# Performance work log

Measured on AMD Instinct MI355X. Metric: run time of the kernel, lower is better.

Reference implementation:

```python
import jax, jax.numpy as jnp
import numpy as np

N_NODES = 50000
N_EDGES = 600000
IN_FEAT = 128
EDGE_DIM = 3
N_HEADS = 4
OUT_FEAT = 32  # per head; N_HEADS*OUT_FEAT == IN_FEAT -> residual_proj is Identity


def setup_inputs() -> dict:
    key = jax.random.key(0)
    ks = jax.random.split(key, 16)
    s = 0.05
    H, F = N_HEADS, OUT_FEAT
    return {
        "node_feats": jax.random.normal(ks[0], (N_NODES, IN_FEAT), jnp.float32),
        "edge_feat": jax.random.normal(ks[1], (N_EDGES, EDGE_DIM), jnp.float32),
        "src": jax.random.randint(ks[2], (N_EDGES,), 0, N_NODES),
        "dst": jax.random.randint(ks[3], (N_EDGES,), 0, N_NODES),
        "W_em1": jax.random.normal(ks[4], (EDGE_DIM, 2 * EDGE_DIM), jnp.float32) * s,
        "b_em1": jnp.zeros((2 * EDGE_DIM,), jnp.float32),
        "W_em2": jax.random.normal(ks[5], (2 * EDGE_DIM, EDGE_DIM), jnp.float32) * s,
        "b_em2": jnp.zeros((EDGE_DIM,), jnp.float32),
        "W_np": jax.random.normal(ks[6], (IN_FEAT, IN_FEAT), jnp.float32) * s,
        "b_np": jnp.zeros((IN_FEAT,), jnp.float32),
        "W_fc": jax.random.normal(ks[7], (IN_FEAT + EDGE_DIM, H * F), jnp.float32) * s,
        "attn_l": jax.random.normal(ks[8], (H, F), jnp.float32) * s,
        "attn_r": jax.random.normal(ks[9], (H, F), jnp.float32) * s,
        "gat_bias": jnp.zeros((H * F,), jnp.float32),
        "ln_gamma": jnp.ones((H * F,), jnp.float32),
        "ln_beta": jnp.zeros((H * F,), jnp.float32),
    }


def reference(node_feats, edge_feat, src, dst, W_em1, b_em1, W_em2, b_em2,
              W_np, b_np, W_fc, attn_l, attn_r, gat_bias, ln_gamma, ln_beta):
    N = node_feats.shape[0]
    H, F = attn_l.shape
    # edge MLP: Linear -> SiLU -> Linear
    e = jax.nn.silu(edge_feat @ W_em1 + b_em1) @ W_em2 + b_em2            # [E, ED]
    p = node_feats @ W_np + b_np                                          # [N, IN]
    src_in = jnp.concatenate([p[src], e], axis=1)                         # [E, IN+ED]
    dst_in = jnp.concatenate([p[dst], e], axis=1)                         # [E, IN+ED]
    temp = jnp.zeros((N, src_in.shape[1]), node_feats.dtype)
    temp = temp.at[src].add(src_in).at[dst].add(dst_in)                   # scatter_add x2
    # GATConv (eval mode: feat_drop/attn_drop are identity)
    h = (temp @ W_fc).reshape(N, H, F)                                    # [N, H, F]
    el = jnp.einsum('nhf,hf->nh', h, attn_l)                              # [N, H]
    er = jnp.einsum('nhf,hf->nh', h, attn_r)                              # [N, H]
    logits = jax.nn.leaky_relu(el[src] + er[dst], negative_slope=0.2)     # [E, H]
    # destination-wise edge softmax (stable)
    m = jax.ops.segment_max(logits, dst, num_segments=N)                  # [N, H]
    a = jnp.exp(logits - m[dst])                                          # [E, H]
    z = jax.ops.segment_sum(a, dst, num_segments=N)                       # [N, H]
    alpha = a / z[dst]                                                    # [E, H]
    msg = alpha[:, :, None] * h[src]                                      # [E, H, F]
    rst = jax.ops.segment_sum(msg, dst, num_segments=N)                   # [N, H, F]
    rst = rst + gat_bias.reshape(1, H, F)
    gat_out = rst.reshape(N, H * F)
    out = gat_out + node_feats                                            # residual (Identity proj)
    mu = out.mean(axis=-1, keepdims=True)
    var = out.var(axis=-1, keepdims=True)
    out = (out - mu) / jnp.sqrt(var + 1e-5) * ln_gamma + ln_beta          # LayerNorm
    return jax.nn.silu(out)
```

## Files before the change

### kernel.cpp

```cpp
#include <hip/hip_runtime.h>
#include <hip/hip_bf16.h>

#define IN_FEAT 128
#define N_HEADS 4
#define OUT_FEAT 32

typedef __attribute__((ext_vector_type(8))) short short8;
typedef __attribute__((ext_vector_type(4))) float floatx4;

__device__ __forceinline__ void bf16split(float x, short& hi, short& lo) {
    unsigned u = __float_as_uint(x);
    unsigned r = (u + 0x7FFFu + ((u >> 16) & 1u)) & 0xFFFF0000u;
    hi = (short)(r >> 16);
    float res = x - __uint_as_float(r);
    unsigned u2 = __float_as_uint(res);
    unsigned r2 = u2 + 0x7FFFu + ((u2 >> 16) & 1u);
    lo = (short)(r2 >> 16);
}

__device__ __forceinline__ unsigned short bf16rne(float x) {
    unsigned u = __float_as_uint(x);
    return (unsigned short)((u + 0x7FFFu + ((u >> 16) & 1u)) >> 16);
}

__global__ void edge_scatter_kernel(const float* __restrict__ ef,
                                    const int* __restrict__ src, const int* __restrict__ dst,
                                    const float* __restrict__ W1, const float* __restrict__ b1,
                                    const float* __restrict__ W2, const float* __restrict__ b2,
                                    float* __restrict__ nd, int* __restrict__ erank, int E) {
    int t = blockIdx.x * blockDim.x + threadIdx.x;
    int e = t >> 3;
    int sub = t & 7;
    if (e >= E) return;
    float x0 = ef[e * 3 + 0], x1 = ef[e * 3 + 1], x2 = ef[e * 3 + 2];
    float hbuf[6];
#pragma unroll
    for (int j = 0; j < 6; j++) {
        float v = x0 * W1[0 * 6 + j] + x1 * W1[1 * 6 + j] + x2 * W1[2 * 6 + j] + b1[j];
        hbuf[j] = v / (1.0f + __expf(-v));
    }
    int j = sub & 3;
    float val;
    if (j == 0) {
        val = 1.0f;
    } else {
        float v = b2[j - 1];
#pragma unroll
        for (int k = 0; k < 6; k++) v += hbuf[k] * W2[k * 3 + (j - 1)];
        val = v;
    }
    int side = sub >> 2;
    int node = side ? dst[e] : src[e];
    int slot = (side && j == 0) ? 4 : j;
    float old = atomicAdd(&nd[(size_t)node * 8 + slot], val);
    if (sub == 4) erank[e] = (int)old;
}

__global__ __launch_bounds__(1024) void scan1_kernel(const float* __restrict__ nd,
                                                     int* __restrict__ excl,
                                                     int* __restrict__ bsum, int N) {
    __shared__ int buf[1024];
    int t = threadIdx.x;
    int i = blockIdx.x * 1024 + t;
    int v = (i < N) ? (int)nd[(size_t)i * 8 + 4] : 0;
    buf[t] = v;
    __syncthreads();
    for (int d = 1; d < 1024; d <<= 1) {
        int x = (t >= d) ? buf[t - d] : 0;
        __syncthreads();
        buf[t] += x;
        __syncthreads();
    }
    if (i < N) excl[i] = buf[t] - v;
    if (t == 1023) bsum[blockIdx.x] = buf[1023];
}

__global__ __launch_bounds__(1024) void scan2_kernel(const int* __restrict__ bsum,
                                                     int* __restrict__ boff, int nb) {
    __shared__ int buf[1024];
    int t = threadIdx.x;
    int v = (t < nb) ? bsum[t] : 0;
    buf[t] = v;
    __syncthreads();
    for (int d = 1; d < 1024; d <<= 1) {
        int x = (t >= d) ? buf[t - d] : 0;
        __syncthreads();
        buf[t] += x;
        __syncthreads();
    }
    if (t < nb) boff[t] = buf[t] - v;
}

__global__ __launch_bounds__(1024) void scan3_kernel(const int* __restrict__ excl,
                                                     const int* __restrict__ boff,
                                                     int* __restrict__ off, int N, int E) {
    int i = blockIdx.x * 1024 + threadIdx.x;
    if (i < N) off[i] = excl[i] + boff[blockIdx.x];
    if (i == 0) off[N] = E;
}

__global__ void wcomb_kernel(const float* __restrict__ W_np, const float* __restrict__ W_fc,
                             const float* __restrict__ b_np,
                             short* __restrict__ WBh, short* __restrict__ WBl,
                             float* __restrict__ bvec) {
    int i = blockIdx.x;
    int o = threadIdx.x;
    float acc = 0.0f;
    for (int j = 0; j < 128; j++) acc += W_np[i * 128 + j] * W_fc[j * 128 + o];
    short hi, lo;
    bf16split(acc, hi, lo);
    int t    = o >> 4;
    int kk   = i >> 5;
    int lane = ((i >> 3) & 3) * 16 + (o & 15);
    int jj   = i & 7;
    int fi = ((t * 4 + kk) * 64 + lane) * 8 + jj;
    WBh[fi] = hi;
    WBl[fi] = lo;
    if (i == 0) {
        float bb = 0.0f;
        for (int j = 0; j < 128; j++) bb += b_np[j] * W_fc[j * 128 + o];
        bvec[o] = bb;
    }
}

__global__ __launch_bounds__(256) void binh_kernel(
        const int* __restrict__ src, const int* __restrict__ dst,
        const int* __restrict__ eoff, const int* __restrict__ erank,
        int* __restrict__ ssrc, int E,
        const float* __restrict__ nf,
        const short* __restrict__ WBh, const short* __restrict__ WBl,
        const float* __restrict__ bvec, const float* __restrict__ W_fc,
        const float* __restrict__ nd,
        const float* __restrict__ attn_l, const float* __restrict__ attn_r,
        unsigned short* __restrict__ h16,
        float* __restrict__ el, float* __restrict__ er, int N) {
    __shared__ short lWh[16384];
    __shared__ short lWl[16384];
    {
        const int4* s1 = (const int4*)WBh;
        const int4* s2 = (const int4*)WBl;
        int4* d1 = (int4*)lWh;
        int4* d2 = (int4*)lWl;
        for (int i = threadIdx.x; i < 2048; i += 256) { d1[i] = s1[i]; d2[i] = s2[i]; }
    }
    __syncthreads();

    {
        int stride = gridDim.x * 256;
#pragma unroll 4
        for (int e = blockIdx.x * 256 + threadIdx.x; e < E; e += stride) {
            ssrc[eoff[dst[e]] + erank[e]] = src[e];
        }
    }

    const int w = threadIdx.x >> 6, l = threadIdx.x & 63;
    const int lrow = l & 15, lhalf = l >> 4;
    const int n0 = blockIdx.x * 64 + w * 16;
    const int arow = n0 + lrow;

    short8 ah[4], al_[4];
#pragma unroll
    for (int kk = 0; kk < 4; kk++) {
        float v[8];
        if (arow < N) {
            const float* p = &nf[(size_t)arow * 128 + kk * 32 + lhalf * 8];
            float4 f0 = *(const float4*)p;
            float4 f1 = *(const float4*)(p + 4);
            v[0] = f0.x; v[1] = f0.y; v[2] = f0.z; v[3] = f0.w;
            v[4] = f1.x; v[5] = f1.y; v[6] = f1.z; v[7] = f1.w;
        } else {
#pragma unroll
            for (int j = 0; j < 8; j++) v[j] = 0.0f;
        }
#pragma unroll
        for (int j = 0; j < 8; j++) {
            short hi, lo;
            bf16split(v[j], hi, lo);
            ah[kk][j] = hi;
            al_[kk][j] = lo;
        }
    }

    floatx4 acc[8];
#pragma unroll
    for (int t = 0; t < 8; t++) acc[t] = (floatx4){0.f, 0.f, 0.f, 0.f};

#pragma unroll
    for (int t = 0; t < 8; t++) {
#pragma unroll
        for (int kk = 0; kk < 4; kk++) {
            int fi = ((t * 4 + kk) * 64 + l) * 8;
            short8 bh = *(const short8*)&lWh[fi];
            short8 bl = *(const short8*)&lWl[fi];
            acc[t] = __builtin_amdgcn_mfma_f32_16x16x32_bf16(ah[kk], bh, acc[t], 0, 0, 0);
            acc[t] = __builtin_amdgcn_mfma_f32_16x16x32_bf16(ah[kk], bl, acc[t], 0, 0, 0);
            acc[t] = __builtin_amdgcn_mfma_f32_16x16x32_bf16(al_[kk], bh, acc[t], 0, 0, 0);
        }
    }

    float bv[8], w0[8], w1[8], w2[8], alb[8], arb[8];
#pragma unroll
    for (int t = 0; t < 8; t++) {
        int o = t * 16 + lrow;
        bv[t] = bvec[o];
        w0[t] = W_fc[128 * 128 + o];
        w1[t] = W_fc[129 * 128 + o];
        w2[t] = W_fc[130 * 128 + o];
        alb[t] = attn_l[o];
        arb[t] = attn_r[o];
    }
#pragma unroll
    for (int r = 0; r < 4; r++) {
        int node = n0 + lhalf * 4 + r;
        bool valid = node < N;
        float dg = 0.f, e0 = 0.f, e1 = 0.f, e2 = 0.f;
        if (valid) {
            dg = nd[(size_t)node * 8 + 0] + nd[(size_t)node * 8 + 4];
            e0 = nd[(size_t)node * 8 + 1];
            e1 = nd[(size_t)node * 8 + 2];
            e2 = nd[(size_t)node * 8 + 3];
        }
        float pl[4] = {0.f, 0.f, 0.f, 0.f}, pr[4] = {0.f, 0.f, 0.f, 0.f};
#pragma unroll
        for (int t = 0; t < 8; t++) {
            float hv = dg * (acc[t][r] + bv[t]) + e0 * w0[t] + e1 * w1[t] + e2 * w2[t];
            if (valid) h16[(size_t)node * 128 + t * 16 + lrow] = bf16rne(hv);
            pl[t >> 1] += hv * alb[t];
            pr[t >> 1] += hv * arb[t];
        }
#pragma unroll
        for (int hd = 0; hd < 4; hd++) {
#pragma unroll
            for (int mask = 1; mask <= 8; mask <<= 1) {
                pl[hd] += __shfl_xor(pl[hd], mask);
                pr[hd] += __shfl_xor(pr[hd], mask);
            }
        }
        if (valid) {
            if (lrow < 4)      el[node * 4 + lrow]       = pl[lrow];
            else if (lrow < 8) er[node * 4 + (lrow - 4)] = pr[lrow - 4];
        }
    }
}

__global__ __launch_bounds__(256) void gather_kernel(
        const int* __restrict__ off, const int* __restrict__ sorted_src,
        const float* __restrict__ el, const float* __restrict__ er,
        const unsigned short* __restrict__ h16, const float* __restrict__ nf,
        const float* __restrict__ gat_bias, const float* __restrict__ gamma,
        const float* __restrict__ beta, float* __restrict__ out, int N) {
    int wid  = (blockIdx.x * blockDim.x + threadIdx.x) >> 6;
    int lane = threadIdx.x & 63;
    int half = lane >> 5;
    int li   = lane & 31;
    int n = wid * 2 + half;
    if (n >= N) return;
    int o0 = li * 4;
    int hd = li >> 3;
    float ern = er[(unsigned)(n * 4 + hd)];
    int beg = off[n], end = off[n + 1];
    float z = 0.f, a0 = 0.f, a1 = 0.f, a2 = 0.f, a3 = 0.f;
    if (beg < end) {
        int s = sorted_src[beg];
        float elv = el[(unsigned)(s * 4 + hd)];
        uint2 hb = *(const uint2*)&h16[(unsigned)(s * 128 + o0)];
        for (int j = beg; j < end; j++) {
            int s2 = (j + 1 < end) ? sorted_src[j + 1] : s;
            float elv2 = el[(unsigned)(s2 * 4 + hd)];
            uint2 hb2 = *(const uint2*)&h16[(unsigned)(s2 * 128 + o0)];
            float l = elv + ern;
            l = (l > 0.f) ? l : 0.2f * l;
            float p = __expf(l);
            z  += p;
            a0 += p * __uint_as_float(hb.x << 16);
            a1 += p * __uint_as_float(hb.x & 0xFFFF0000u);
            a2 += p * __uint_as_float(hb.y << 16);
            a3 += p * __uint_as_float(hb.y & 0xFFFF0000u);
            elv = elv2; hb = hb2; s = s2;
        }
    }
    float izv = (end > beg) ? 1.0f / z : 0.f;
    float4 nfv = *(const float4*)&nf[(size_t)n * 128 + o0];
    float v0 = a0 * izv + gat_bias[o0]     + nfv.x;
    float v1 = a1 * izv + gat_bias[o0 + 1] + nfv.y;
    float v2 = a2 * izv + gat_bias[o0 + 2] + nfv.z;
    float v3 = a3 * izv + gat_bias[o0 + 3] + nfv.w;
    float s  = v0 + v1 + v2 + v3;
    float s2 = v0 * v0 + v1 * v1 + v2 * v2 + v3 * v3;
#pragma unroll
    for (int mask = 1; mask <= 16; mask <<= 1) {
        s  += __shfl_xor(s, mask);
        s2 += __shfl_xor(s2, mask);
    }
    float mu = s * (1.0f / 128.0f);
    float var = s2 * (1.0f / 128.0f) - mu * mu;
    float inv = rsqrtf(var + 1e-5f);
    float y0 = (v0 - mu) * inv * gamma[o0]     + beta[o0];
    float y1 = (v1 - mu) * inv * gamma[o0 + 1] + beta[o0 + 1];
    float y2 = (v2 - mu) * inv * gamma[o0 + 2] + beta[o0 + 2];
    float y3 = (v3 - mu) * inv * gamma[o0 + 3] + beta[o0 + 3];
    float4 ov;
    ov.x = y0 / (1.0f + __expf(-y0));
    ov.y = y1 / (1.0f + __expf(-y1));
    ov.z = y2 / (1.0f + __expf(-y2));
    ov.w = y3 / (1.0f + __expf(-y3));
    *(float4*)&out[(size_t)n * 128 + o0] = ov;
}

extern "C" void kernel_launch(void* const* d_in, const int* in_sizes, int n_in,
                              void* d_out, int out_size, void* d_ws, size_t ws_size,
                              hipStream_t stream) {
    const float* nf     = (const float*)d_in[0];
    const float* ef     = (const float*)d_in[1];
    const int*   src    = (const int*)d_in[2];
    const int*   dst    = (const int*)d_in[3];
    const float* W_em1  = (const float*)d_in[4];
    const float* b_em1  = (const float*)d_in[5];
    const float* W_em2  = (const float*)d_in[6];
    const float* b_em2  = (const float*)d_in[7];
    const float* W_np   = (const float*)d_in[8];
    const float* b_np   = (const float*)d_in[9];
    const float* W_fc   = (const float*)d_in[10];
    const float* attn_l = (const float*)d_in[11];
    const float* attn_r = (const float*)d_in[12];
    const float* g_bias = (const float*)d_in[13];
    const float* ln_g   = (const float*)d_in[14];
    const float* ln_b   = (const float*)d_in[15];

    const int N = in_sizes[0] / IN_FEAT;
    const int E = in_sizes[2];

    float* ws = (float*)d_ws;
    size_t off_w = 0;
    auto alloc = [&](size_t nelem) {
        float* p = ws + off_w;
        off_w += (nelem + 63) & ~(size_t)63;
        return p;
    };
    float* nd    = alloc((size_t)N * 8);
    short* WBh   = (short*)alloc(128 * 128 / 2);
    short* WBl   = (short*)alloc(128 * 128 / 2);
    float* bvec  = alloc(128);
    unsigned short* h16 = (unsigned short*)alloc((size_t)N * 64);
    float* el    = alloc((size_t)N * 4);
    float* er    = alloc((size_t)N * 4);
    int*   erank  = (int*)alloc(E);
    int*   eoff   = (int*)alloc(N + 1);
    int*   ssrc   = (int*)alloc(E);
    int*   excl   = (int*)alloc(N);
    int*   bsum   = (int*)alloc(1024);
    int*   boff   = (int*)alloc(1024);

    const int nb = (N + 1023) / 1024;

    hipMemsetAsync(nd, 0, (size_t)N * 8 * sizeof(float), stream);

    edge_scatter_kernel<<<((size_t)E * 8 + 255) / 256, 256, 0, stream>>>(
        ef, src, dst, W_em1, b_em1, W_em2, b_em2, nd, erank, E);
    wcomb_kernel<<<128, 128, 0, stream>>>(W_np, W_fc, b_np, WBh, WBl, bvec);
    scan1_kernel<<<nb, 1024, 0, stream>>>(nd, excl, bsum, N);
    scan2_kernel<<<1, 1024, 0, stream>>>(bsum, boff, nb);
    scan3_kernel<<<nb, 1024, 0, stream>>>(excl, boff, eoff, N, E);
    binh_kernel<<<(N + 63) / 64, 256, 0, stream>>>(src, dst, eoff, erank, ssrc, E,
                                                   nf, WBh, WBl, bvec, W_fc, nd,
                                                   attn_l, attn_r, h16, el, er, N);
    gather_kernel<<<((size_t)N * 32 + 255) / 256, 256, 0, stream>>>(eoff, ssrc, el, er, h16, nf,
                                                                    g_bias, ln_g, ln_b,
                                                                    (float*)d_out, N);
}
```

Before: 156.5 us.

## Fuse scan passes, fold memset into wcomb, drop LDS staging and split term

Removes the separate scan2 kernel by having each scan3 block sum the preceding block totals serially, and replaces the hipMemsetAsync of the node accumulator with a zeroing loop inside wcomb_kernel, which now launches before edge_scatter. In binh_kernel the weight staging into shared memory is removed so B fragments are read directly from global memory, and the activation low-part bf16 MFMA term is dropped, cutting MFMA work by a third. The aim is fewer launches and less per-block setup, at the cost of lower precision in the node projection and repeated global/L2 weight reads.

```diff
diff --git a/kernel.cpp b/kernel.cpp
--- a/kernel.cpp
+++ b/kernel.cpp
@@ -75,34 +75,29 @@
     if (t == 1023) bsum[blockIdx.x] = buf[1023];
 }
 
-__global__ __launch_bounds__(1024) void scan2_kernel(const int* __restrict__ bsum,
-                                                     int* __restrict__ boff, int nb) {
-    __shared__ int buf[1024];
-    int t = threadIdx.x;
-    int v = (t < nb) ? bsum[t] : 0;
-    buf[t] = v;
+__global__ __launch_bounds__(1024) void scan3_kernel(const int* __restrict__ excl,
+                                                     const int* __restrict__ bsum,
+                                                     int* __restrict__ off, int N, int E) {
+    __shared__ int base;
+    if (threadIdx.x == 0) {
+        int s = 0;
+        for (int k = 0; k < (int)blockIdx.x; k++) s += bsum[k];
+        base = s;
+    }
     __syncthreads();
-    for (int d = 1; d < 1024; d <<= 1) {
-        int x = (t >= d) ? buf[t - d] : 0;
-        __syncthreads();
-        buf[t] += x;
-        __syncthreads();
-    }
-    if (t < nb) boff[t] = buf[t] - v;
-}
-
-__global__ __launch_bounds__(1024) void scan3_kernel(const int* __restrict__ excl,
-                                                     const int* __restrict__ boff,
-                                                     int* __restrict__ off, int N, int E) {
     int i = blockIdx.x * 1024 + threadIdx.x;
-    if (i < N) off[i] = excl[i] + boff[blockIdx.x];
+    if (i < N) off[i] = excl[i] + base;
     if (i == 0) off[N] = E;
 }
 
 __global__ void wcomb_kernel(const float* __restrict__ W_np, const float* __restrict__ W_fc,
                              const float* __restrict__ b_np,
                              short* __restrict__ WBh, short* __restrict__ WBl,
-                             float* __restrict__ bvec) {
+                             float* __restrict__ bvec,
+                             float4* __restrict__ ndz, int zcnt) {
+    for (int i = blockIdx.x * blockDim.x + threadIdx.x; i < zcnt; i += gridDim.x * blockDim.x)
+        ndz[i] = (float4){0.f, 0.f, 0.f, 0.f};
+
     int i = blockIdx.x;
     int o = threadIdx.x;
     float acc = 0.0f;
@@ -134,20 +129,8 @@
         const float* __restrict__ attn_l, const float* __restrict__ attn_r,
         unsigned short* __restrict__ h16,
         float* __restrict__ el, float* __restrict__ er, int N) {
-    __shared__ short lWh[16384];
-    __shared__ short lWl[16384];
-    {
-        const int4* s1 = (const int4*)WBh;
-        const int4* s2 = (const int4*)WBl;
-        int4* d1 = (int4*)lWh;
-        int4* d2 = (int4*)lWl;
-        for (int i = threadIdx.x; i < 2048; i += 256) { d1[i] = s1[i]; d2[i] = s2[i]; }
-    }
-    __syncthreads();
-
     {
         int stride = gridDim.x * 256;
-#pragma unroll 4
         for (int e = blockIdx.x * 256 + threadIdx.x; e < E; e += stride) {
             ssrc[eoff[dst[e]] + erank[e]] = src[e];
         }
@@ -158,7 +141,7 @@
     const int n0 = blockIdx.x * 64 + w * 16;
     const int arow = n0 + lrow;
 
-    short8 ah[4], al_[4];
+    short8 ah[4];
 #pragma unroll
     for (int kk = 0; kk < 4; kk++) {
         float v[8];
@@ -173,28 +156,22 @@
             for (int j = 0; j < 8; j++) v[j] = 0.0f;
         }
 #pragma unroll
-        for (int j = 0; j < 8; j++) {
-            short hi, lo;
-            bf16split(v[j], hi, lo);
-            ah[kk][j] = hi;
-            al_[kk][j] = lo;
-        }
-    }
-
+        for (int j = 0; j < 8; j++) ah[kk][j] = (short)bf16rne(v[j]);
+    }
+
+    const short8* gbh = (const short8*)WBh;
+    const short8* gbl = (const short8*)WBl;
     floatx4 acc[8];
 #pragma unroll
     for (int t = 0; t < 8; t++) acc[t] = (floatx4){0.f, 0.f, 0.f, 0.f};
-
 #pragma unroll
     for (int t = 0; t < 8; t++) {
 #pragma unroll
         for (int kk = 0; kk < 4; kk++) {
-            int fi = ((t * 4 + kk) * 64 + l) * 8;
-            short8 bh = *(const short8*)&lWh[fi];
-            short8 bl = *(const short8*)&lWl[fi];
+            short8 bh = gbh[(t * 4 + kk) * 64 + l];
+            short8 bl = gbl[(t * 4 + kk) * 64 + l];
             acc[t] = __builtin_amdgcn_mfma_f32_16x16x32_bf16(ah[kk], bh, acc[t], 0, 0, 0);
             acc[t] = __builtin_amdgcn_mfma_f32_16x16x32_bf16(ah[kk], bl, acc[t], 0, 0, 0);
-            acc[t] = __builtin_amdgcn_mfma_f32_16x16x32_bf16(al_[kk], bh, acc[t], 0, 0, 0);
         }
     }
 
@@ -349,18 +326,15 @@
     int*   ssrc   = (int*)alloc(E);
     int*   excl   = (int*)alloc(N);
     int*   bsum   = (int*)alloc(1024);
-    int*   boff   = (int*)alloc(1024);
 
     const int nb = (N + 1023) / 1024;
 
-    hipMemsetAsync(nd, 0, (size_t)N * 8 * sizeof(float), stream);
-
+    wcomb_kernel<<<128, 128, 0, stream>>>(W_np, W_fc, b_np, WBh, WBl, bvec,
+                                          (float4*)nd, N * 2);
     edge_scatter_kernel<<<((size_t)E * 8 + 255) / 256, 256, 0, stream>>>(
         ef, src, dst, W_em1, b_em1, W_em2, b_em2, nd, erank, E);
-    wcomb_kernel<<<128, 128, 0, stream>>>(W_np, W_fc, b_np, WBh, WBl, bvec);
     scan1_kernel<<<nb, 1024, 0, stream>>>(nd, excl, bsum, N);
-    scan2_kernel<<<1, 1024, 0, stream>>>(bsum, boff, nb);
-    scan3_kernel<<<nb, 1024, 0, stream>>>(excl, boff, eoff, N, E);
+    scan3_kernel<<<nb, 1024, 0, stream>>>(excl, bsum, eoff, N, E);
     binh_kernel<<<(N + 63) / 64, 256, 0, stream>>>(src, dst, eoff, erank, ssrc, E,
                                                    nf, WBh, WBl, bvec, W_fc, nd,
                                                    attn_l, attn_r, h16, el, er, N);
```

Result: faster. 151.4 us (-3.3%).
